# Optimization experiments

Measured on AMD Instinct MI355X. Metric: run time of the kernel, lower is better.

## Reference

```python
import jax, jax.numpy as jnp
import numpy as np
import math

N_ENTITIES = 200000
N_ITEMS = 100000
N_REL = 40
DIM = 64
N_HEADS = 2
DK = DIM // N_HEADS
N_EDGES = 1500000
K_EDGES = 256
K_ITEMS = 100


def setup_inputs() -> dict:
    key = jax.random.key(0)
    k1, k2, k3, k4, k5, k6 = jax.random.split(key, 6)
    entity_emb = jax.random.normal(k1, (N_ENTITIES, DIM), jnp.float32) * 0.1
    W_Q = jax.random.normal(k2, (DIM, DIM), jnp.float32) * (1.0 / math.sqrt(DIM))
    relation_emb = jax.random.normal(k3, (N_REL - 1, DIM), jnp.float32) * 0.1
    edge_index = jax.random.randint(k4, (2, N_EDGES), 0, N_ENTITIES, jnp.int32)
    # edge_type in [1, N_REL-1]: code indexes relation_emb[edge_type - 1]
    edge_type = jax.random.randint(k5, (N_EDGES,), 1, N_REL, jnp.int32)
    # uniform(0,1) driving the gumbel noise -log(-log(u)); clipped away from 0
    noise_u = jax.random.uniform(k6, (N_EDGES,), jnp.float32, 1e-9, 1.0)
    return {"entity_emb": entity_emb, "W_Q": W_Q, "relation_emb": relation_emb,
            "noise_u": noise_u, "edge_index": edge_index, "edge_type": edge_type}


def reference(entity_emb, W_Q, relation_emb, noise_u, edge_index, edge_type):
    head, tail = edge_index[0], edge_index[1]
    E = edge_index.shape[1]

    # --- norm_attn_computer (AttnHGCN): per-edge multi-head attention ---
    # project once on nodes, then gather (same math as (emb[head] @ W_Q))
    proj = entity_emb @ W_Q                               # [N, D]
    q = proj[head].reshape(E, N_HEADS, DK)                # [E, H, Dk]
    k = proj[tail].reshape(E, N_HEADS, DK)                # [E, H, Dk]
    rel = relation_emb[edge_type - 1].reshape(E, N_HEADS, DK)
    attn = jnp.sum(q * k * rel, axis=-1) / math.sqrt(DK)  # [E, H]
    edge_attn_logits = attn.mean(axis=-1)                 # [E]

    # scatter_softmax over head nodes, then multiply by head degree (norm)
    seg_max = jax.lax.stop_gradient(
        jax.ops.segment_max(edge_attn_logits, head, num_segments=N_ENTITIES))
    ex = jnp.exp(edge_attn_logits - seg_max[head])
    denom = jax.ops.segment_sum(ex, head, num_segments=N_ENTITIES)
    edge_attn_score = ex / denom[head]
    deg = jax.ops.segment_sum(jnp.ones_like(edge_attn_logits), head,
                              num_segments=N_ENTITIES)
    edge_attn_score = edge_attn_score * deg[head]         # [E]

    # --- attn logit sums per item (head + tail scatter_sum), topk 100 ---
    sum_by_node = (jax.ops.segment_sum(edge_attn_logits, head, num_segments=N_ENTITIES)
                   + jax.ops.segment_sum(edge_attn_logits, tail, num_segments=N_ENTITIES))
    top_items_v, top_attn_items = jax.lax.top_k(sum_by_node[:N_ITEMS], K_ITEMS)

    # --- gumbel-noise injection + edge topk 256 ---
    noisy_score = edge_attn_score + (-jnp.log(-jnp.log(noise_u)))
    topk_v, topk_attn_edge_id = jax.lax.top_k(noisy_score, K_EDGES)

    return (edge_attn_score, topk_v, topk_attn_edge_id, top_items_v, top_attn_items)
```

## Files before the change

### kernel.cpp

```cpp
#include <hip/hip_runtime.h>

#define N_ENTITIES 200000
#define N_ITEMS    100000
#define DIM        64
#define N_EDGES    1500000
#define K_EDGES    256
#define K_ITEMS    100
#define SCALE      0.08838834764831845f

#define CAND_CAP   8192
#define NBLK3      1024
#define NB1        256
#define EPB        5860
#define NBUCK      782
#define NSC        (NBUCK * NB1)
#define L2CAP      2816

typedef unsigned long long u64;


__device__ __forceinline__ unsigned fkey(float x) {
    unsigned u = __float_as_uint(x);
    return (u & 0x80000000u) ? ~u : (u | 0x80000000u);
}
__device__ __forceinline__ float funkey(unsigned k) {
    return (k & 0x80000000u) ? __uint_as_float(k & 0x7fffffffu)
                             : __uint_as_float(~k);
}

__device__ __forceinline__ unsigned select_digit(const unsigned* __restrict__ hist,
                                                 unsigned Keff, unsigned* above) {
    unsigned cum = 0;
    int b = 255;
    for (; b > 0; --b) {
        unsigned hb = hist[b];
        if (cum + hb >= Keff) break;
        cum += hb;
    }
    *above = cum;
    return (unsigned)b;
}

__global__ __launch_bounds__(256) void proj_kernel(const float* __restrict__ emb,
                                                   const float* __restrict__ W,
                                                   float* __restrict__ proj) {
    __shared__ float part[4][16][64];
    const int t = threadIdx.x;
    const int c = t & 63;
    const int q = __builtin_amdgcn_readfirstlane(t >> 6);

    float Wreg[16];
#pragma unroll
    for (int j = 0; j < 16; ++j) Wreg[j] = W[(q * 16 + j) * 64 + c];

    const int base = blockIdx.x * 16;
    const float* erow = emb + (size_t)base * 64 + q * 16;

    float acc[16];
#pragma unroll
    for (int r = 0; r < 16; ++r) acc[r] = 0.f;
#pragma unroll
    for (int r = 0; r < 16; ++r) {
#pragma unroll
        for (int j = 0; j < 16; ++j)
            acc[r] += erow[r * 64 + j] * Wreg[j];
    }
#pragma unroll
    for (int r = 0; r < 16; ++r) part[q][r][c] = acc[r];
    __syncthreads();
#pragma unroll
    for (int it = 0; it < 4; ++it) {
        int oi = t + it * 256;
        int r = oi >> 6, cc = oi & 63;
        float s = part[0][r][cc] + part[1][r][cc] + part[2][r][cc] + part[3][r][cc];
        proj[(size_t)(base + r) * 64 + cc] = s;
    }
}

__global__ __launch_bounds__(256) void bhist_kernel(const int* __restrict__ head,
                                                    unsigned* __restrict__ off) {
    __shared__ unsigned lh[NBUCK];
    for (int k = threadIdx.x; k < NBUCK; k += 256) lh[k] = 0;
    __syncthreads();
    int base = blockIdx.x * EPB;
    int end = base + EPB; if (end > N_EDGES) end = N_EDGES;
    for (int e = base + threadIdx.x; e < end; e += 256)
        atomicAdd(&lh[(unsigned)head[e] >> 8], 1u);
    __syncthreads();
    for (int k = threadIdx.x; k < NBUCK; k += 256)
        off[(size_t)k * NB1 + blockIdx.x] = lh[k];
}

__global__ void scanA_kernel(unsigned* __restrict__ a, unsigned* __restrict__ bsum) {
    __shared__ unsigned s[256];
    int t = threadIdx.x, i = blockIdx.x * 256 + t;
    unsigned v = a[i];
    s[t] = v;
    __syncthreads();
    for (int off = 1; off < 256; off <<= 1) {
        unsigned x = s[t];
        unsigned y = (t >= off) ? s[t - off] : 0u;
        __syncthreads();
        s[t] = x + y;
        __syncthreads();
    }
    a[i] = s[t] - v;
    if (t == 255) bsum[blockIdx.x] = s[t];
}
__global__ __launch_bounds__(256) void scanB_kernel(const unsigned* __restrict__ bsum,
                                                    unsigned* __restrict__ a) {
    __shared__ unsigned part[4];
    const int b = blockIdx.x;
    const int t = threadIdx.x;
    unsigned s = 0;
    for (int j = t; j < b; j += 256) s += bsum[j];
#pragma unroll
    for (int off = 1; off < 64; off <<= 1) s += __shfl_xor(s, off, 64);
    if ((t & 63) == 0) part[t >> 6] = s;
    __syncthreads();
    unsigned prefix = part[0] + part[1] + part[2] + part[3];
    a[b * 256 + t] += prefix;
}

__global__ __launch_bounds__(256) void bscat_kernel(const int* __restrict__ head,
                                                    const int* __restrict__ tail,
                                                    const int* __restrict__ etype,
                                                    const unsigned* __restrict__ off,
                                                    u64* __restrict__ rec2) {
    __shared__ unsigned lh[NBUCK];
    __shared__ unsigned loff[NBUCK];
    for (int k = threadIdx.x; k < NBUCK; k += 256) {
        lh[k] = 0;
        loff[k] = off[(size_t)k * NB1 + blockIdx.x];
    }
    __syncthreads();
    int base = blockIdx.x * EPB;
    int end = base + EPB; if (end > N_EDGES) end = N_EDGES;
    for (int e = base + threadIdx.x; e < end; e += 256) {
        unsigned h = (unsigned)head[e];
        unsigned bkt = h >> 8;
        unsigned r = atomicAdd(&lh[bkt], 1u);
        u64 R = ((u64)h << 45) | ((u64)(unsigned)tail[e] << 27)
              | ((u64)(unsigned)(etype[e] - 1) << 21) | (u64)(unsigned)e;
        rec2[loff[bkt] + r] = R;
    }
}

__global__ __launch_bounds__(256) void csr_kernel(const u64* __restrict__ rec2,
                                                  const unsigned* __restrict__ off,
                                                  u64* __restrict__ rec3,
                                                  unsigned* __restrict__ start,
                                                  unsigned* __restrict__ degtot) {
    __shared__ u64 srec[L2CAP];
    __shared__ u64 sdst[L2CAP];
    __shared__ unsigned short srank[L2CAP];
    __shared__ unsigned lh[256];
    __shared__ unsigned lscan[256];
    const int bkt = blockIdx.x;
    const unsigned gstart = off[(size_t)bkt * NB1];
    const unsigned gend = (bkt == NBUCK - 1) ? (unsigned)N_EDGES
                                             : off[(size_t)(bkt + 1) * NB1];
    unsigned n = gend - gstart;
    if (n > L2CAP) n = L2CAP;
    lh[threadIdx.x] = 0;
    __syncthreads();
    for (unsigned j = threadIdx.x; j < n; j += 256) {
        u64 R = rec2[gstart + j];
        srec[j] = R;
        unsigned hl = (unsigned)(R >> 45) & 255u;
        srank[j] = (unsigned short)atomicAdd(&lh[hl], 1u);
    }
    __syncthreads();
    unsigned v = lh[threadIdx.x];
    lscan[threadIdx.x] = v;
    __syncthreads();
    for (int o = 1; o < 256; o <<= 1) {
        unsigned x = lscan[threadIdx.x];
        unsigned y = (threadIdx.x >= o) ? lscan[threadIdx.x - o] : 0u;
        __syncthreads();
        lscan[threadIdx.x] = x + y;
        __syncthreads();
    }
    unsigned excl = lscan[threadIdx.x] - v;
    __syncthreads();
    lscan[threadIdx.x] = excl;
    const int h0 = bkt * 256;
    const int entCount = (N_ENTITIES - h0 < 256) ? (N_ENTITIES - h0) : 256;
    if ((int)threadIdx.x < entCount) {
        start[h0 + threadIdx.x] = gstart + excl;
        degtot[h0 + threadIdx.x] = v;
    }
    __syncthreads();
    for (unsigned j = threadIdx.x; j < n; j += 256) {
        u64 R = srec[j];
        unsigned hl = (unsigned)(R >> 45) & 255u;
        sdst[lscan[hl] + srank[j]] = R;
    }
    __syncthreads();
    for (unsigned j = threadIdx.x; j < n; j += 256) rec3[gstart + j] = sdst[j];
}

__global__ __launch_bounds__(256) void node_pass(const float4* __restrict__ proj4,
                                                 const float4* __restrict__ rel4,
                                                 const u64* __restrict__ rec,
                                                 const unsigned* __restrict__ start,
                                                 const unsigned* __restrict__ degtot,
                                                 float* __restrict__ logits,
                                                 float2* __restrict__ nd,
                                                 float* __restrict__ sumhead,
                                                 float* __restrict__ sumI) {
    int wave = (blockIdx.x * blockDim.x + threadIdx.x) >> 6;
    int lane = threadIdx.x & 63;
    int slot = lane >> 4, sl = lane & 15;
    unsigned s = start[wave], len = degtot[wave];
    float4 ph = proj4[(size_t)wave * 16 + sl];
    float dsum = 0.f, lsum = 0.f;
    for (unsigned k0 = 0; k0 < len; k0 += 8) {
        unsigned ka = k0 + slot, kb = ka + 4;
        bool va = (ka < len), vb = (kb < len);
        u64 Ra = rec[s + (va ? ka : 0u)];
        u64 Rb = rec[s + (vb ? kb : 0u)];
        unsigned ta = (unsigned)(Ra >> 27) & 0x3FFFFu, ria = ((unsigned)(Ra >> 21)) & 63u;
        unsigned tb = (unsigned)(Rb >> 27) & 0x3FFFFu, rib = ((unsigned)(Rb >> 21)) & 63u;
        unsigned ea = (unsigned)Ra & 0x1FFFFFu, eb = (unsigned)Rb & 0x1FFFFFu;
        float4 pa = proj4[(size_t)ta * 16 + sl];
        float4 qa = rel4[(size_t)ria * 16 + sl];
        float4 pb = proj4[(size_t)tb * 16 + sl];
        float4 qb = rel4[(size_t)rib * 16 + sl];
        float xa = ph.x * pa.x * qa.x + ph.y * pa.y * qa.y + ph.z * pa.z * qa.z + ph.w * pa.w * qa.w;
        float xb = ph.x * pb.x * qb.x + ph.y * pb.y * qb.y + ph.z * pb.z * qb.z + ph.w * pb.w * qb.w;
        xa += __shfl_xor(xa, 1, 64);  xb += __shfl_xor(xb, 1, 64);
        xa += __shfl_xor(xa, 2, 64);  xb += __shfl_xor(xb, 2, 64);
        xa += __shfl_xor(xa, 4, 64);  xb += __shfl_xor(xb, 4, 64);
        xa += __shfl_xor(xa, 8, 64);  xb += __shfl_xor(xb, 8, 64);
        if (sl == 0) {
            if (va) {
                float lg = xa * SCALE;
                logits[ea] = lg;
                dsum += __expf(lg);
                lsum += lg;
                if (ta < N_ITEMS) atomicAdd(&sumI[ta], lg);
            }
            if (vb) {
                float lg = xb * SCALE;
                logits[eb] = lg;
                dsum += __expf(lg);
                lsum += lg;
                if (tb < N_ITEMS) atomicAdd(&sumI[tb], lg);
            }
        }
    }
    dsum += __shfl_xor(dsum, 16, 64);
    dsum += __shfl_xor(dsum, 32, 64);
    lsum += __shfl_xor(lsum, 16, 64);
    lsum += __shfl_xor(lsum, 32, 64);
    if (lane == 0) {
        nd[wave] = make_float2(dsum, (float)len);
        sumhead[wave] = lsum;
    }
}

__global__ __launch_bounds__(256) void edge_pass3(const float* __restrict__ logits,
                           const int* __restrict__ head,
                           const float2* __restrict__ nd, const float* __restrict__ noise_u,
                           const float* __restrict__ sumhead, const float* __restrict__ sumI,
                           float* __restrict__ out_scores, unsigned* __restrict__ keysE,
                           unsigned* __restrict__ keysI, unsigned* __restrict__ histB) {
    __shared__ unsigned hh[512];
    for (int j = threadIdx.x; j < 512; j += blockDim.x) hh[j] = 0;
    __syncthreads();

    const int stride = NBLK3 * 256;
    for (int i = blockIdx.x * blockDim.x + threadIdx.x; i < N_EDGES; i += stride) {
        float lg = logits[i];
        float2 dd = nd[head[i]];
        float score = __expf(lg) / dd.x * dd.y;
        out_scores[i] = score;
        float noise = -logf(-logf(noise_u[i]));
        unsigned k = fkey(score + noise);
        keysE[i] = k;
        atomicAdd(&hh[k >> 24], 1u);
        if (i < N_ITEMS) {
            unsigned ki = fkey(sumhead[i] + sumI[i]);
            keysI[i] = ki;
            atomicAdd(&hh[256 + (ki >> 24)], 1u);
        }
    }
    __syncthreads();
    unsigned* row = histB + (size_t)blockIdx.x * 512;
    for (int j = threadIdx.x; j < 512; j += blockDim.x) row[j] = hh[j];
}

__global__ void reduce_hist_kernel(const unsigned* __restrict__ histB,
                                   unsigned* __restrict__ hists) {
    const int bin = blockIdx.x;
    unsigned s = 0;
    for (int r = threadIdx.x; r < NBLK3; r += 64)
        s += histB[(size_t)r * 512 + bin];
#pragma unroll
    for (int off = 1; off < 64; off <<= 1) s += __shfl_xor(s, off, 64);
    if (threadIdx.x == 0) hists[bin] = s;
}

__global__ void collect_kernel(const unsigned* __restrict__ keysE,
                               const unsigned* __restrict__ keysI,
                               const unsigned* __restrict__ hists,
                               unsigned* __restrict__ counters, unsigned* __restrict__ cand) {
    const int y = blockIdx.y;
    const unsigned* keys = y ? keysI : keysE;
    const int n = y ? N_ITEMS : N_EDGES;
    const unsigned K = y ? K_ITEMS : K_EDGES;
    const unsigned* H = hists + (size_t)y * 256;
    unsigned aboveA;
    unsigned binA = select_digit(H, K, &aboveA);
    const unsigned T = binA << 24;
    unsigned* cd = cand + (size_t)y * 2 * CAND_CAP;

    int i = blockIdx.x * blockDim.x + threadIdx.x;
    int stride = gridDim.x * blockDim.x;
    for (; i < n; i += stride) {
        unsigned k = keys[i];
        if (k >= T) {
            unsigned p = atomicAdd(&counters[y], 1u);
            if (p < (unsigned)CAND_CAP) { cd[2 * p] = k; cd[2 * p + 1] = (unsigned)i; }
        }
    }
}

__global__ void final_topk_kernel(const unsigned* __restrict__ cand,
                                  const unsigned* __restrict__ counters,
                                  float* __restrict__ out_topkv, float* __restrict__ out_topki,
                                  float* __restrict__ out_itemv, float* __restrict__ out_itemi) {
    __shared__ unsigned sk[CAND_CAP];
    __shared__ unsigned si[CAND_CAP];
    const int y = blockIdx.x;
    const int K = y ? K_ITEMS : K_EDGES;
    float* outv = y ? out_itemv : out_topkv;
    float* outi = y ? out_itemi : out_topki;
    const unsigned* cd = cand + (size_t)y * 2 * CAND_CAP;
    unsigned m = counters[y];
    if (m > (unsigned)CAND_CAP) m = CAND_CAP;
    for (unsigned i = threadIdx.x; i < m; i += blockDim.x) {
        sk[i] = cd[2 * i];
        si[i] = cd[2 * i + 1];
    }
    __syncthreads();
    for (unsigned i = threadIdx.x; i < m; i += blockDim.x) {
        unsigned ki = sk[i], xi = si[i];
        int r = 0;
        for (unsigned j = 0; j < m; ++j) {
            unsigned kj = sk[j];
            if (kj > ki || (kj == ki && si[j] < xi)) r++;
        }
        if (r < K) {
            outv[r] = funkey(ki);
            outi[r] = (float)xi;
        }
    }
}

extern "C" void kernel_launch(void* const* d_in, const int* in_sizes, int n_in,
                              void* d_out, int out_size, void* d_ws, size_t ws_size,
                              hipStream_t stream) {
    (void)in_sizes; (void)n_in; (void)out_size; (void)ws_size;
    const float* emb    = (const float*)d_in[0];
    const float* W      = (const float*)d_in[1];
    const float* rel    = (const float*)d_in[2];
    const float* noise  = (const float*)d_in[3];
    const int*   eidx   = (const int*)d_in[4];
    const int*   etype  = (const int*)d_in[5];
    const int* head = eidx;
    const int* tail = eidx + N_EDGES;

    float* out        = (float*)d_out;
    float* out_scores = out;
    float* out_topkv  = out + N_EDGES;
    float* out_topki  = out + N_EDGES + K_EDGES;
    float* out_itemv  = out + N_EDGES + 2 * K_EDGES;
    float* out_itemi  = out + N_EDGES + 2 * K_EDGES + K_ITEMS;

    float* ws = (float*)d_ws;
    size_t o = 0;
    float*    proj    = ws + o;               o += (size_t)N_ENTITIES * DIM;
    unsigned* off     = (unsigned*)(ws + o);  o += NSC;
    unsigned* bsum    = (unsigned*)(ws + o);  o += 1024;
    u64*      rec2    = (u64*)(ws + o);       o += 2 * (size_t)N_EDGES;
    u64*      rec3    = (u64*)(ws + o);       o += 2 * (size_t)N_EDGES;
    unsigned* keysE   = (unsigned*)rec2;
    unsigned* keysI   = keysE + N_EDGES;
    unsigned* start   = (unsigned*)(ws + o);  o += N_ENTITIES;
    unsigned* degtot  = (unsigned*)(ws + o);  o += N_ENTITIES;
    float*    logits  = ws + o;               o += N_EDGES;
    float2*   nd      = (float2*)(ws + o);    o += 2 * (size_t)N_ENTITIES;
    float*    sumhead = ws + o;               o += N_ENTITIES;
    float*    sumI    = ws + o;               o += N_ITEMS;
    unsigned* counters= (unsigned*)(ws + o);  o += 2;
    unsigned* histB   = (unsigned*)(ws + o);  o += (size_t)NBLK3 * 512;
    unsigned* hists   = (unsigned*)(ws + o);  o += 512;
    unsigned* cand    = (unsigned*)(ws + o);  o += 2 * 2 * CAND_CAP;

    hipMemsetAsync(sumI, 0, ((size_t)N_ITEMS + 2) * 4, stream);
    hipLaunchKernelGGL(proj_kernel, dim3(12500), dim3(256), 0, stream, emb, W, proj);
    hipLaunchKernelGGL(bhist_kernel, dim3(NB1), dim3(256), 0, stream, head, off);
    hipLaunchKernelGGL(scanA_kernel, dim3(NSC / 256), dim3(256), 0, stream, off, bsum);
    hipLaunchKernelGGL(scanB_kernel, dim3(NSC / 256), dim3(256), 0, stream, bsum, off);
    hipLaunchKernelGGL(bscat_kernel, dim3(NB1), dim3(256), 0, stream,
                       head, tail, etype, off, rec2);
    hipLaunchKernelGGL(csr_kernel, dim3(NBUCK), dim3(256), 0, stream,
                       rec2, off, rec3, start, degtot);
    hipLaunchKernelGGL(node_pass, dim3(N_ENTITIES / 4), dim3(256), 0, stream,
                       (const float4*)proj, (const float4*)rel, rec3, start, degtot,
                       logits, nd, sumhead, sumI);
    hipLaunchKernelGGL(edge_pass3, dim3(NBLK3), dim3(256), 0, stream,
                       logits, head, nd, noise, sumhead, sumI,
                       out_scores, keysE, keysI, histB);
    hipLaunchKernelGGL(reduce_hist_kernel, dim3(512), dim3(64), 0, stream, histB, hists);
    hipLaunchKernelGGL(collect_kernel, dim3(512, 2), dim3(256), 0, stream,
                       keysE, keysI, hists, counters, cand);
    hipLaunchKernelGGL(final_topk_kernel, dim3(2), dim3(1024), 0, stream,
                       cand, counters, out_topkv, out_topki, out_itemv, out_itemi);
}
```

Baseline: 437.1 us.

## Fuse post-projection pipeline into one persistent kernel with grid barriers

Nine separate kernels (bucket histogram, scans, scatter, CSR build, node pass, edge pass, histogram reduce, collect, final top-k) are merged into a single persistent kernel sized to fill the device, with software grid-wide barriers between phases. Per-block histograms are now reduced with global atomics instead of a separate reduce kernel. Shared memory is shrunk to a fixed 1920-word buffer, so the CSR phase no longer stages full buckets in LDS, and the final top-k reads candidates from global memory across 16 blocks. The goal is to remove launch overhead and inter-kernel gaps. The cost is spin-barrier latency, reduced parallelism in phases that had many small blocks, and a risk of deadlock if not all blocks are co-resident.

```diff
diff --git a/kernel.cpp b/kernel.cpp
--- a/kernel.cpp
+++ b/kernel.cpp
@@ -9,7 +9,6 @@
 #define SCALE      0.08838834764831845f
 
 #define CAND_CAP   8192
-#define NBLK3      1024
 #define NB1        256
 #define EPB        5860
 #define NBUCK      782
@@ -41,6 +40,27 @@
     return (unsigned)b;
 }
 
+__device__ __forceinline__ void gbar(unsigned* bar) {
+    __syncthreads();
+    if (threadIdx.x == 0) {
+        __builtin_amdgcn_fence(__ATOMIC_RELEASE, "agent");
+        unsigned gen = __hip_atomic_load(&bar[1], __ATOMIC_RELAXED, __HIP_MEMORY_SCOPE_AGENT);
+        unsigned a = __hip_atomic_fetch_add(&bar[0], 1u, __ATOMIC_RELAXED, __HIP_MEMORY_SCOPE_AGENT);
+        if (a == gridDim.x - 1) {
+            __hip_atomic_store(&bar[0], 0u, __ATOMIC_RELAXED, __HIP_MEMORY_SCOPE_AGENT);
+            __hip_atomic_store(&bar[1], gen + 1u, __ATOMIC_RELAXED, __HIP_MEMORY_SCOPE_AGENT);
+        } else {
+            unsigned long long spins = 0;
+            while (__hip_atomic_load(&bar[1], __ATOMIC_RELAXED, __HIP_MEMORY_SCOPE_AGENT) == gen) {
+                __builtin_amdgcn_s_sleep(2);
+                if (++spins > 60000000ull) break;
+            }
+        }
+        __builtin_amdgcn_fence(__ATOMIC_ACQUIRE, "agent");
+    }
+    __syncthreads();
+}
+
 __global__ __launch_bounds__(256) void proj_kernel(const float* __restrict__ emb,
                                                    const float* __restrict__ W,
                                                    float* __restrict__ proj) {
@@ -77,284 +97,271 @@
     }
 }
 
-__global__ __launch_bounds__(256) void bhist_kernel(const int* __restrict__ head,
-                                                    unsigned* __restrict__ off) {
-    __shared__ unsigned lh[NBUCK];
-    for (int k = threadIdx.x; k < NBUCK; k += 256) lh[k] = 0;
-    __syncthreads();
-    int base = blockIdx.x * EPB;
-    int end = base + EPB; if (end > N_EDGES) end = N_EDGES;
-    for (int e = base + threadIdx.x; e < end; e += 256)
-        atomicAdd(&lh[(unsigned)head[e] >> 8], 1u);
-    __syncthreads();
-    for (int k = threadIdx.x; k < NBUCK; k += 256)
-        off[(size_t)k * NB1 + blockIdx.x] = lh[k];
-}
-
-__global__ void scanA_kernel(unsigned* __restrict__ a, unsigned* __restrict__ bsum) {
-    __shared__ unsigned s[256];
-    int t = threadIdx.x, i = blockIdx.x * 256 + t;
-    unsigned v = a[i];
-    s[t] = v;
-    __syncthreads();
-    for (int off = 1; off < 256; off <<= 1) {
-        unsigned x = s[t];
-        unsigned y = (t >= off) ? s[t - off] : 0u;
-        __syncthreads();
-        s[t] = x + y;
-        __syncthreads();
-    }
-    a[i] = s[t] - v;
-    if (t == 255) bsum[blockIdx.x] = s[t];
-}
-__global__ __launch_bounds__(256) void scanB_kernel(const unsigned* __restrict__ bsum,
-                                                    unsigned* __restrict__ a) {
-    __shared__ unsigned part[4];
-    const int b = blockIdx.x;
+__global__ __launch_bounds__(256) void mega_kernel(
+    const int* __restrict__ head, const int* __restrict__ tailp,
+    const int* __restrict__ etype,
+    const float4* __restrict__ proj4, const float4* __restrict__ rel4,
+    const float* __restrict__ noise_u,
+    unsigned* __restrict__ off, unsigned* __restrict__ rowtot,
+    u64* __restrict__ rec2, u64* __restrict__ rec3,
+    unsigned* __restrict__ start, unsigned* __restrict__ degtot,
+    float* __restrict__ logits, float2* __restrict__ nd,
+    float* __restrict__ sumhead, float* __restrict__ sumI,
+    float* __restrict__ out_scores,
+    unsigned* __restrict__ keysE, unsigned* __restrict__ keysI,
+    unsigned* __restrict__ hists, unsigned* __restrict__ counters,
+    unsigned* __restrict__ cand,
+    float* __restrict__ out_topkv, float* __restrict__ out_topki,
+    float* __restrict__ out_itemv, float* __restrict__ out_itemi,
+    unsigned* __restrict__ bar)
+{
+    __shared__ unsigned smem[1920];
     const int t = threadIdx.x;
-    unsigned s = 0;
-    for (int j = t; j < b; j += 256) s += bsum[j];
-#pragma unroll
-    for (int off = 1; off < 64; off <<= 1) s += __shfl_xor(s, off, 64);
-    if ((t & 63) == 0) part[t >> 6] = s;
-    __syncthreads();
-    unsigned prefix = part[0] + part[1] + part[2] + part[3];
-    a[b * 256 + t] += prefix;
-}
-
-__global__ __launch_bounds__(256) void bscat_kernel(const int* __restrict__ head,
-                                                    const int* __restrict__ tail,
-                                                    const int* __restrict__ etype,
-                                                    const unsigned* __restrict__ off,
-                                                    u64* __restrict__ rec2) {
-    __shared__ unsigned lh[NBUCK];
-    __shared__ unsigned loff[NBUCK];
-    for (int k = threadIdx.x; k < NBUCK; k += 256) {
-        lh[k] = 0;
-        loff[k] = off[(size_t)k * NB1 + blockIdx.x];
-    }
-    __syncthreads();
-    int base = blockIdx.x * EPB;
-    int end = base + EPB; if (end > N_EDGES) end = N_EDGES;
-    for (int e = base + threadIdx.x; e < end; e += 256) {
-        unsigned h = (unsigned)head[e];
-        unsigned bkt = h >> 8;
-        unsigned r = atomicAdd(&lh[bkt], 1u);
-        u64 R = ((u64)h << 45) | ((u64)(unsigned)tail[e] << 27)
-              | ((u64)(unsigned)(etype[e] - 1) << 21) | (u64)(unsigned)e;
-        rec2[loff[bkt] + r] = R;
-    }
-}
-
-__global__ __launch_bounds__(256) void csr_kernel(const u64* __restrict__ rec2,
-                                                  const unsigned* __restrict__ off,
-                                                  u64* __restrict__ rec3,
-                                                  unsigned* __restrict__ start,
-                                                  unsigned* __restrict__ degtot) {
-    __shared__ u64 srec[L2CAP];
-    __shared__ u64 sdst[L2CAP];
-    __shared__ unsigned short srank[L2CAP];
-    __shared__ unsigned lh[256];
-    __shared__ unsigned lscan[256];
-    const int bkt = blockIdx.x;
-    const unsigned gstart = off[(size_t)bkt * NB1];
-    const unsigned gend = (bkt == NBUCK - 1) ? (unsigned)N_EDGES
-                                             : off[(size_t)(bkt + 1) * NB1];
-    unsigned n = gend - gstart;
-    if (n > L2CAP) n = L2CAP;
-    lh[threadIdx.x] = 0;
-    __syncthreads();
-    for (unsigned j = threadIdx.x; j < n; j += 256) {
-        u64 R = rec2[gstart + j];
-        srec[j] = R;
-        unsigned hl = (unsigned)(R >> 45) & 255u;
-        srank[j] = (unsigned short)atomicAdd(&lh[hl], 1u);
-    }
-    __syncthreads();
-    unsigned v = lh[threadIdx.x];
-    lscan[threadIdx.x] = v;
-    __syncthreads();
-    for (int o = 1; o < 256; o <<= 1) {
-        unsigned x = lscan[threadIdx.x];
-        unsigned y = (threadIdx.x >= o) ? lscan[threadIdx.x - o] : 0u;
-        __syncthreads();
-        lscan[threadIdx.x] = x + y;
-        __syncthreads();
-    }
-    unsigned excl = lscan[threadIdx.x] - v;
-    __syncthreads();
-    lscan[threadIdx.x] = excl;
-    const int h0 = bkt * 256;
-    const int entCount = (N_ENTITIES - h0 < 256) ? (N_ENTITIES - h0) : 256;
-    if ((int)threadIdx.x < entCount) {
-        start[h0 + threadIdx.x] = gstart + excl;
-        degtot[h0 + threadIdx.x] = v;
-    }
-    __syncthreads();
-    for (unsigned j = threadIdx.x; j < n; j += 256) {
-        u64 R = srec[j];
-        unsigned hl = (unsigned)(R >> 45) & 255u;
-        sdst[lscan[hl] + srank[j]] = R;
-    }
-    __syncthreads();
-    for (unsigned j = threadIdx.x; j < n; j += 256) rec3[gstart + j] = sdst[j];
-}
-
-__global__ __launch_bounds__(256) void node_pass(const float4* __restrict__ proj4,
-                                                 const float4* __restrict__ rel4,
-                                                 const u64* __restrict__ rec,
-                                                 const unsigned* __restrict__ start,
-                                                 const unsigned* __restrict__ degtot,
-                                                 float* __restrict__ logits,
-                                                 float2* __restrict__ nd,
-                                                 float* __restrict__ sumhead,
-                                                 float* __restrict__ sumI) {
-    int wave = (blockIdx.x * blockDim.x + threadIdx.x) >> 6;
-    int lane = threadIdx.x & 63;
-    int slot = lane >> 4, sl = lane & 15;
-    unsigned s = start[wave], len = degtot[wave];
-    float4 ph = proj4[(size_t)wave * 16 + sl];
-    float dsum = 0.f, lsum = 0.f;
-    for (unsigned k0 = 0; k0 < len; k0 += 8) {
-        unsigned ka = k0 + slot, kb = ka + 4;
-        bool va = (ka < len), vb = (kb < len);
-        u64 Ra = rec[s + (va ? ka : 0u)];
-        u64 Rb = rec[s + (vb ? kb : 0u)];
-        unsigned ta = (unsigned)(Ra >> 27) & 0x3FFFFu, ria = ((unsigned)(Ra >> 21)) & 63u;
-        unsigned tb = (unsigned)(Rb >> 27) & 0x3FFFFu, rib = ((unsigned)(Rb >> 21)) & 63u;
-        unsigned ea = (unsigned)Ra & 0x1FFFFFu, eb = (unsigned)Rb & 0x1FFFFFu;
-        float4 pa = proj4[(size_t)ta * 16 + sl];
-        float4 qa = rel4[(size_t)ria * 16 + sl];
-        float4 pb = proj4[(size_t)tb * 16 + sl];
-        float4 qb = rel4[(size_t)rib * 16 + sl];
-        float xa = ph.x * pa.x * qa.x + ph.y * pa.y * qa.y + ph.z * pa.z * qa.z + ph.w * pa.w * qa.w;
-        float xb = ph.x * pb.x * qb.x + ph.y * pb.y * qb.y + ph.z * pb.z * qb.z + ph.w * pb.w * qb.w;
-        xa += __shfl_xor(xa, 1, 64);  xb += __shfl_xor(xb, 1, 64);
-        xa += __shfl_xor(xa, 2, 64);  xb += __shfl_xor(xb, 2, 64);
-        xa += __shfl_xor(xa, 4, 64);  xb += __shfl_xor(xb, 4, 64);
-        xa += __shfl_xor(xa, 8, 64);  xb += __shfl_xor(xb, 8, 64);
-        if (sl == 0) {
-            if (va) {
-                float lg = xa * SCALE;
-                logits[ea] = lg;
-                dsum += __expf(lg);
-                lsum += lg;
-                if (ta < N_ITEMS) atomicAdd(&sumI[ta], lg);
-            }
-            if (vb) {
-                float lg = xb * SCALE;
-                logits[eb] = lg;
-                dsum += __expf(lg);
-                lsum += lg;
-                if (tb < N_ITEMS) atomicAdd(&sumI[tb], lg);
-            }
-        }
-    }
-    dsum += __shfl_xor(dsum, 16, 64);
-    dsum += __shfl_xor(dsum, 32, 64);
-    lsum += __shfl_xor(lsum, 16, 64);
-    lsum += __shfl_xor(lsum, 32, 64);
-    if (lane == 0) {
-        nd[wave] = make_float2(dsum, (float)len);
-        sumhead[wave] = lsum;
-    }
-}
-
-__global__ __launch_bounds__(256) void edge_pass3(const float* __restrict__ logits,
-                           const int* __restrict__ head,
-                           const float2* __restrict__ nd, const float* __restrict__ noise_u,
-                           const float* __restrict__ sumhead, const float* __restrict__ sumI,
-                           float* __restrict__ out_scores, unsigned* __restrict__ keysE,
-                           unsigned* __restrict__ keysI, unsigned* __restrict__ histB) {
-    __shared__ unsigned hh[512];
-    for (int j = threadIdx.x; j < 512; j += blockDim.x) hh[j] = 0;
-    __syncthreads();
-
-    const int stride = NBLK3 * 256;
-    for (int i = blockIdx.x * blockDim.x + threadIdx.x; i < N_EDGES; i += stride) {
-        float lg = logits[i];
-        float2 dd = nd[head[i]];
-        float score = __expf(lg) / dd.x * dd.y;
-        out_scores[i] = score;
-        float noise = -logf(-logf(noise_u[i]));
-        unsigned k = fkey(score + noise);
-        keysE[i] = k;
-        atomicAdd(&hh[k >> 24], 1u);
-        if (i < N_ITEMS) {
-            unsigned ki = fkey(sumhead[i] + sumI[i]);
-            keysI[i] = ki;
-            atomicAdd(&hh[256 + (ki >> 24)], 1u);
-        }
-    }
-    __syncthreads();
-    unsigned* row = histB + (size_t)blockIdx.x * 512;
-    for (int j = threadIdx.x; j < 512; j += blockDim.x) row[j] = hh[j];
-}
-
-__global__ void reduce_hist_kernel(const unsigned* __restrict__ histB,
-                                   unsigned* __restrict__ hists) {
-    const int bin = blockIdx.x;
-    unsigned s = 0;
-    for (int r = threadIdx.x; r < NBLK3; r += 64)
-        s += histB[(size_t)r * 512 + bin];
-#pragma unroll
-    for (int off = 1; off < 64; off <<= 1) s += __shfl_xor(s, off, 64);
-    if (threadIdx.x == 0) hists[bin] = s;
-}
-
-__global__ void collect_kernel(const unsigned* __restrict__ keysE,
-                               const unsigned* __restrict__ keysI,
-                               const unsigned* __restrict__ hists,
-                               unsigned* __restrict__ counters, unsigned* __restrict__ cand) {
-    const int y = blockIdx.y;
-    const unsigned* keys = y ? keysI : keysE;
-    const int n = y ? N_ITEMS : N_EDGES;
-    const unsigned K = y ? K_ITEMS : K_EDGES;
-    const unsigned* H = hists + (size_t)y * 256;
-    unsigned aboveA;
-    unsigned binA = select_digit(H, K, &aboveA);
-    const unsigned T = binA << 24;
-    unsigned* cd = cand + (size_t)y * 2 * CAND_CAP;
-
-    int i = blockIdx.x * blockDim.x + threadIdx.x;
-    int stride = gridDim.x * blockDim.x;
-    for (; i < n; i += stride) {
-        unsigned k = keys[i];
-        if (k >= T) {
-            unsigned p = atomicAdd(&counters[y], 1u);
-            if (p < (unsigned)CAND_CAP) { cd[2 * p] = k; cd[2 * p + 1] = (unsigned)i; }
-        }
-    }
-}
-
-__global__ void final_topk_kernel(const unsigned* __restrict__ cand,
-                                  const unsigned* __restrict__ counters,
-                                  float* __restrict__ out_topkv, float* __restrict__ out_topki,
-                                  float* __restrict__ out_itemv, float* __restrict__ out_itemi) {
-    __shared__ unsigned sk[CAND_CAP];
-    __shared__ unsigned si[CAND_CAP];
-    const int y = blockIdx.x;
-    const int K = y ? K_ITEMS : K_EDGES;
-    float* outv = y ? out_itemv : out_topkv;
-    float* outi = y ? out_itemi : out_topki;
-    const unsigned* cd = cand + (size_t)y * 2 * CAND_CAP;
-    unsigned m = counters[y];
-    if (m > (unsigned)CAND_CAP) m = CAND_CAP;
-    for (unsigned i = threadIdx.x; i < m; i += blockDim.x) {
-        sk[i] = cd[2 * i];
-        si[i] = cd[2 * i + 1];
-    }
-    __syncthreads();
-    for (unsigned i = threadIdx.x; i < m; i += blockDim.x) {
-        unsigned ki = sk[i], xi = si[i];
-        int r = 0;
-        for (unsigned j = 0; j < m; ++j) {
-            unsigned kj = sk[j];
-            if (kj > ki || (kj == ki && si[j] < xi)) r++;
-        }
-        if (r < K) {
-            outv[r] = funkey(ki);
-            outi[r] = (float)xi;
+    const int G = gridDim.x;
+
+    for (int vb = blockIdx.x; vb < NB1; vb += G) {
+        for (int j = t; j < NBUCK; j += 256) smem[j] = 0;
+        __syncthreads();
+        int base = vb * EPB;
+        int end = base + EPB; if (end > N_EDGES) end = N_EDGES;
+        for (int e = base + t; e < end; e += 256)
+            atomicAdd(&smem[(unsigned)head[e] >> 8], 1u);
+        __syncthreads();
+        for (int j = t; j < NBUCK; j += 256)
+            off[(size_t)j * NB1 + vb] = smem[j];
+        __syncthreads();
+    }
+    gbar(bar);
+
+    for (int k = blockIdx.x; k < NBUCK; k += G) {
+        unsigned v = off[(size_t)k * NB1 + t];
+        smem[t] = v;
+        __syncthreads();
+        for (int o = 1; o < 256; o <<= 1) {
+            unsigned x = smem[t];
+            unsigned y = (t >= o) ? smem[t - o] : 0u;
+            __syncthreads();
+            smem[t] = x + y;
+            __syncthreads();
+        }
+        off[(size_t)k * NB1 + t] = smem[t] - v;
+        if (t == 255) rowtot[k] = smem[t];
+        __syncthreads();
+    }
+    gbar(bar);
+
+    for (int k = blockIdx.x; k < NBUCK; k += G) {
+        unsigned s = 0;
+        for (int j = t; j < k; j += 256) s += rowtot[j];
+#pragma unroll
+        for (int o = 1; o < 64; o <<= 1) s += __shfl_xor(s, o, 64);
+        if ((t & 63) == 0) smem[256 + (t >> 6)] = s;
+        __syncthreads();
+        unsigned prefix = smem[256] + smem[257] + smem[258] + smem[259];
+        off[(size_t)k * NB1 + t] += prefix;
+        __syncthreads();
+    }
+    gbar(bar);
+
+    for (int vb = blockIdx.x; vb < NB1; vb += G) {
+        unsigned* lh = smem;
+        unsigned* loff = smem + NBUCK;
+        for (int j = t; j < NBUCK; j += 256) {
+            lh[j] = 0;
+            loff[j] = off[(size_t)j * NB1 + vb];
+        }
+        __syncthreads();
+        int base = vb * EPB;
+        int end = base + EPB; if (end > N_EDGES) end = N_EDGES;
+        for (int e = base + t; e < end; e += 256) {
+            unsigned h = (unsigned)head[e];
+            unsigned bkt = h >> 8;
+            unsigned r = atomicAdd(&lh[bkt], 1u);
+            u64 R = ((u64)h << 45) | ((u64)(unsigned)tailp[e] << 27)
+                  | ((u64)(unsigned)(etype[e] - 1) << 21) | (u64)(unsigned)e;
+            rec2[loff[bkt] + r] = R;
+        }
+        __syncthreads();
+    }
+    gbar(bar);
+
+    for (int bkt = blockIdx.x; bkt < NBUCK; bkt += G) {
+        unsigned* lh = smem;
+        unsigned* lscan = smem + 256;
+        unsigned short* srank = (unsigned short*)(smem + 512);
+        const unsigned gstart = off[(size_t)bkt * NB1];
+        const unsigned gend = (bkt == NBUCK - 1) ? (unsigned)N_EDGES
+                                                 : off[(size_t)(bkt + 1) * NB1];
+        unsigned n = gend - gstart;
+        if (n > L2CAP) n = L2CAP;
+        lh[t] = 0;
+        __syncthreads();
+        for (unsigned j = t; j < n; j += 256) {
+            u64 R = rec2[gstart + j];
+            unsigned hl = (unsigned)(R >> 45) & 255u;
+            srank[j] = (unsigned short)atomicAdd(&lh[hl], 1u);
+        }
+        __syncthreads();
+        unsigned v = lh[t];
+        lscan[t] = v;
+        __syncthreads();
+        for (int o = 1; o < 256; o <<= 1) {
+            unsigned x = lscan[t];
+            unsigned y = (t >= o) ? lscan[t - o] : 0u;
+            __syncthreads();
+            lscan[t] = x + y;
+            __syncthreads();
+        }
+        unsigned excl = lscan[t] - v;
+        __syncthreads();
+        lscan[t] = excl;
+        const int h0 = bkt * 256;
+        const int entCount = (N_ENTITIES - h0 < 256) ? (N_ENTITIES - h0) : 256;
+        if (t < entCount) {
+            start[h0 + t] = gstart + excl;
+            degtot[h0 + t] = v;
+        }
+        __syncthreads();
+        for (unsigned j = t; j < n; j += 256) {
+            u64 R = rec2[gstart + j];
+            unsigned hl = (unsigned)(R >> 45) & 255u;
+            rec3[gstart + lscan[hl] + srank[j]] = R;
+        }
+        __syncthreads();
+    }
+    gbar(bar);
+
+    {
+        const int wid = (blockIdx.x * 256 + t) >> 6;
+        const int W = G * 4;
+        const int lane = t & 63;
+        const int slot = lane >> 4, sl = lane & 15;
+        for (int node = wid; node < N_ENTITIES; node += W) {
+            unsigned s = start[node], len = degtot[node];
+            float4 ph = proj4[(size_t)node * 16 + sl];
+            float dsum = 0.f, lsum = 0.f;
+            for (unsigned k0 = 0; k0 < len; k0 += 8) {
+                unsigned ka = k0 + slot, kb = ka + 4;
+                bool va = (ka < len), vb = (kb < len);
+                u64 Ra = rec3[s + (va ? ka : 0u)];
+                u64 Rb = rec3[s + (vb ? kb : 0u)];
+                unsigned ta = (unsigned)(Ra >> 27) & 0x3FFFFu, ria = ((unsigned)(Ra >> 21)) & 63u;
+                unsigned tb = (unsigned)(Rb >> 27) & 0x3FFFFu, rib = ((unsigned)(Rb >> 21)) & 63u;
+                unsigned ea = (unsigned)Ra & 0x1FFFFFu, eb = (unsigned)Rb & 0x1FFFFFu;
+                float4 pa = proj4[(size_t)ta * 16 + sl];
+                float4 qa = rel4[(size_t)ria * 16 + sl];
+                float4 pb = proj4[(size_t)tb * 16 + sl];
+                float4 qb = rel4[(size_t)rib * 16 + sl];
+                float xa = ph.x * pa.x * qa.x + ph.y * pa.y * qa.y
+                         + ph.z * pa.z * qa.z + ph.w * pa.w * qa.w;
+                float xb = ph.x * pb.x * qb.x + ph.y * pb.y * qb.y
+                         + ph.z * pb.z * qb.z + ph.w * pb.w * qb.w;
+                xa += __shfl_xor(xa, 1, 64);  xb += __shfl_xor(xb, 1, 64);
+                xa += __shfl_xor(xa, 2, 64);  xb += __shfl_xor(xb, 2, 64);
+                xa += __shfl_xor(xa, 4, 64);  xb += __shfl_xor(xb, 4, 64);
+                xa += __shfl_xor(xa, 8, 64);  xb += __shfl_xor(xb, 8, 64);
+                if (sl == 0) {
+                    if (va) {
+                        float lg = xa * SCALE;
+                        logits[ea] = lg;
+                        dsum += __expf(lg);
+                        lsum += lg;
+                        if (ta < N_ITEMS) atomicAdd(&sumI[ta], lg);
+                    }
+                    if (vb) {
+                        float lg = xb * SCALE;
+                        logits[eb] = lg;
+                        dsum += __expf(lg);
+                        lsum += lg;
+                        if (tb < N_ITEMS) atomicAdd(&sumI[tb], lg);
+                    }
+                }
+            }
+            dsum += __shfl_xor(dsum, 16, 64);
+            dsum += __shfl_xor(dsum, 32, 64);
+            lsum += __shfl_xor(lsum, 16, 64);
+            lsum += __shfl_xor(lsum, 32, 64);
+            if (lane == 0) {
+                nd[node] = make_float2(dsum, (float)len);
+                sumhead[node] = lsum;
+            }
+        }
+    }
+    gbar(bar);
+
+    {
+        unsigned* hh = smem;
+        for (int j = t; j < 512; j += 256) hh[j] = 0;
+        __syncthreads();
+        const int stride = G * 256;
+        for (int i = blockIdx.x * 256 + t; i < N_EDGES; i += stride) {
+            float lg = logits[i];
+            float2 dd = nd[head[i]];
+            float score = __expf(lg) / dd.x * dd.y;
+            out_scores[i] = score;
+            float noise = -logf(-logf(noise_u[i]));
+            unsigned k = fkey(score + noise);
+            keysE[i] = k;
+            atomicAdd(&hh[k >> 24], 1u);
+            if (i < N_ITEMS) {
+                unsigned ki = fkey(sumhead[i] + sumI[i]);
+                keysI[i] = ki;
+                atomicAdd(&hh[256 + (ki >> 24)], 1u);
+            }
+        }
+        __syncthreads();
+        for (int j = t; j < 512; j += 256) {
+            unsigned v = hh[j];
+            if (v) atomicAdd(&hists[j], v);
+        }
+    }
+    gbar(bar);
+
+    {
+        const int stride = G * 256;
+        unsigned aboveA;
+        unsigned binA = select_digit(hists, K_EDGES, &aboveA);
+        unsigned T = binA << 24;
+        for (int i = blockIdx.x * 256 + t; i < N_EDGES; i += stride) {
+            unsigned k = keysE[i];
+            if (k >= T) {
+                unsigned p = atomicAdd(&counters[0], 1u);
+                if (p < (unsigned)CAND_CAP) { cand[2 * p] = k; cand[2 * p + 1] = (unsigned)i; }
+            }
+        }
+        binA = select_digit(hists + 256, K_ITEMS, &aboveA);
+        T = binA << 24;
+        unsigned* cd = cand + 2 * CAND_CAP;
+        for (int i = blockIdx.x * 256 + t; i < N_ITEMS; i += stride) {
+            unsigned k = keysI[i];
+            if (k >= T) {
+                unsigned p = atomicAdd(&counters[1], 1u);
+                if (p < (unsigned)CAND_CAP) { cd[2 * p] = k; cd[2 * p + 1] = (unsigned)i; }
+            }
+        }
+    }
+    gbar(bar);
+
+    if (blockIdx.x < 16) {
+        const int y = blockIdx.x >> 3;
+        const int sub = blockIdx.x & 7;
+        const int K = y ? K_ITEMS : K_EDGES;
+        float* outv = y ? out_itemv : out_topkv;
+        float* outi = y ? out_itemi : out_topki;
+        const unsigned* cd = cand + (size_t)y * 2 * CAND_CAP;
+        unsigned m = counters[y];
+        if (m > (unsigned)CAND_CAP) m = CAND_CAP;
+        for (unsigned i = sub * 256 + t; i < m; i += 2048) {
+            unsigned ki = cd[2 * i], xi = cd[2 * i + 1];
+            int r = 0;
+            for (unsigned j = 0; j < m; ++j) {
+                unsigned kj = cd[2 * j];
+                if (kj > ki || (kj == ki && cd[2 * j + 1] < xi)) r++;
+            }
+            if (r < K) {
+                outv[r] = funkey(ki);
+                outi[r] = (float)xi;
+            }
         }
     }
 }
@@ -383,7 +390,7 @@
     size_t o = 0;
     float*    proj    = ws + o;               o += (size_t)N_ENTITIES * DIM;
     unsigned* off     = (unsigned*)(ws + o);  o += NSC;
-    unsigned* bsum    = (unsigned*)(ws + o);  o += 1024;
+    unsigned* rowtot  = (unsigned*)(ws + o);  o += 1024;
     u64*      rec2    = (u64*)(ws + o);       o += 2 * (size_t)N_EDGES;
     u64*      rec3    = (u64*)(ws + o);       o += 2 * (size_t)N_EDGES;
     unsigned* keysE   = (unsigned*)rec2;
@@ -394,29 +401,33 @@
     float2*   nd      = (float2*)(ws + o);    o += 2 * (size_t)N_ENTITIES;
     float*    sumhead = ws + o;               o += N_ENTITIES;
     float*    sumI    = ws + o;               o += N_ITEMS;
+    unsigned* hists   = (unsigned*)(ws + o);  o += 512;
     unsigned* counters= (unsigned*)(ws + o);  o += 2;
-    unsigned* histB   = (unsigned*)(ws + o);  o += (size_t)NBLK3 * 512;
-    unsigned* hists   = (unsigned*)(ws + o);  o += 512;
+    unsigned* bar     = (unsigned*)(ws + o);  o += 16;
     unsigned* cand    = (unsigned*)(ws + o);  o += 2 * 2 * CAND_CAP;
 
-    hipMemsetAsync(sumI, 0, ((size_t)N_ITEMS + 2) * 4, stream);
+    static int G = 0;
+    if (G == 0) {
+        int dev = 0;
+        hipGetDevice(&dev);
+        hipDeviceProp_t prop;
+        int cus = 256;
+        if (hipGetDeviceProperties(&prop, dev) == hipSuccess) cus = prop.multiProcessorCount;
+        int occ = 0;
+        if (hipOccupancyMaxActiveBlocksPerMultiprocessor(&occ, mega_kernel, 256, 0) != hipSuccess
+            || occ < 1) occ = 1;
+        G = occ * cus;
+        if (G < 16) G = 16;
+        if (G > 4096) G = 4096;
+    }
+
+    hipMemsetAsync(sumI, 0, ((size_t)N_ITEMS + 512 + 2 + 16) * 4, stream);
     hipLaunchKernelGGL(proj_kernel, dim3(12500), dim3(256), 0, stream, emb, W, proj);
-    hipLaunchKernelGGL(bhist_kernel, dim3(NB1), dim3(256), 0, stream, head, off);
-    hipLaunchKernelGGL(scanA_kernel, dim3(NSC / 256), dim3(256), 0, stream, off, bsum);
-    hipLaunchKernelGGL(scanB_kernel, dim3(NSC / 256), dim3(256), 0, stream, bsum, off);
-    hipLaunchKernelGGL(bscat_kernel, dim3(NB1), dim3(256), 0, stream,
-                       head, tail, etype, off, rec2);
-    hipLaunchKernelGGL(csr_kernel, dim3(NBUCK), dim3(256), 0, stream,
-                       rec2, off, rec3, start, degtot);
-    hipLaunchKernelGGL(node_pass, dim3(N_ENTITIES / 4), dim3(256), 0, stream,
-                       (const float4*)proj, (const float4*)rel, rec3, start, degtot,
-                       logits, nd, sumhead, sumI);
-    hipLaunchKernelGGL(edge_pass3, dim3(NBLK3), dim3(256), 0, stream,
-                       logits, head, nd, noise, sumhead, sumI,
-                       out_scores, keysE, keysI, histB);
-    hipLaunchKernelGGL(reduce_hist_kernel, dim3(512), dim3(64), 0, stream, histB, hists);
-    hipLaunchKernelGGL(collect_kernel, dim3(512, 2), dim3(256), 0, stream,
-                       keysE, keysI, hists, counters, cand);
-    hipLaunchKernelGGL(final_topk_kernel, dim3(2), dim3(1024), 0, stream,
-                       cand, counters, out_topkv, out_topki, out_itemv, out_itemi);
-}
+    hipLaunchKernelGGL(mega_kernel, dim3(G), dim3(256), 0, stream,
+                       head, tail, etype,
+                       (const float4*)proj, (const float4*)rel, noise,
+                       off, rowtot, rec2, rec3, start, degtot,
+                       logits, nd, sumhead, sumI,
+                       out_scores, keysE, keysI, hists, counters, cand,
+                       out_topkv, out_topki, out_itemv, out_itemi, bar);
+}
```

After: 1.466 ms. +235.5%, slower.

## Fuse CSR bucket sort with node attention pass and atomically reduce histograms

Applied to the files above, without the earlier changes.

Shrinks head-node buckets from 256 to 64 nodes so each bucket fits in LDS. The CSR sort and the per-node attention pass are merged into one kernel that reads sorted edge records directly from shared memory, which removes the rec3, start and degtot global round trips and one kernel launch. The per-block histogram array and its reduce kernel are replaced by atomic adds into a global histogram that is zeroed alongside sumI. In exchange, per-bucket capacity drops to 768 edges (overflow is silently truncated), each 256-thread block now processes 64 nodes serially across 4 waves, the bucket scatter has four times as many buckets, and the histogram relies on contended global atomics.

```diff
diff --git a/kernel.cpp b/kernel.cpp
--- a/kernel.cpp
+++ b/kernel.cpp
@@ -12,9 +12,10 @@
 #define NBLK3      1024
 #define NB1        256
 #define EPB        5860
-#define NBUCK      782
+#define BSH        6
+#define NBUCK      3125
 #define NSC        (NBUCK * NB1)
-#define L2CAP      2816
+#define L2CAP      768
 
 typedef unsigned long long u64;
 
@@ -85,7 +86,7 @@
     int base = blockIdx.x * EPB;
     int end = base + EPB; if (end > N_EDGES) end = N_EDGES;
     for (int e = base + threadIdx.x; e < end; e += 256)
-        atomicAdd(&lh[(unsigned)head[e] >> 8], 1u);
+        atomicAdd(&lh[(unsigned)head[e] >> BSH], 1u);
     __syncthreads();
     for (int k = threadIdx.x; k < NBUCK; k += 256)
         off[(size_t)k * NB1 + blockIdx.x] = lh[k];
@@ -138,7 +139,7 @@
     int end = base + EPB; if (end > N_EDGES) end = N_EDGES;
     for (int e = base + threadIdx.x; e < end; e += 256) {
         unsigned h = (unsigned)head[e];
-        unsigned bkt = h >> 8;
+        unsigned bkt = h >> BSH;
         unsigned r = atomicAdd(&lh[bkt], 1u);
         u64 R = ((u64)h << 45) | ((u64)(unsigned)tail[e] << 27)
               | ((u64)(unsigned)(etype[e] - 1) << 21) | (u64)(unsigned)e;
@@ -146,117 +147,107 @@
     }
 }
 
-__global__ __launch_bounds__(256) void csr_kernel(const u64* __restrict__ rec2,
-                                                  const unsigned* __restrict__ off,
-                                                  u64* __restrict__ rec3,
-                                                  unsigned* __restrict__ start,
-                                                  unsigned* __restrict__ degtot) {
-    __shared__ u64 srec[L2CAP];
+__global__ __launch_bounds__(256) void csrnode_kernel(const u64* __restrict__ rec2,
+                                                      const unsigned* __restrict__ off,
+                                                      const float4* __restrict__ proj4,
+                                                      const float4* __restrict__ rel4,
+                                                      float* __restrict__ logits,
+                                                      float2* __restrict__ nd,
+                                                      float* __restrict__ sumhead,
+                                                      float* __restrict__ sumI) {
     __shared__ u64 sdst[L2CAP];
     __shared__ unsigned short srank[L2CAP];
-    __shared__ unsigned lh[256];
-    __shared__ unsigned lscan[256];
+    __shared__ unsigned lh[64];
+    __shared__ unsigned lscan[64];
+    const int t = threadIdx.x;
     const int bkt = blockIdx.x;
     const unsigned gstart = off[(size_t)bkt * NB1];
     const unsigned gend = (bkt == NBUCK - 1) ? (unsigned)N_EDGES
                                              : off[(size_t)(bkt + 1) * NB1];
     unsigned n = gend - gstart;
     if (n > L2CAP) n = L2CAP;
-    lh[threadIdx.x] = 0;
-    __syncthreads();
-    for (unsigned j = threadIdx.x; j < n; j += 256) {
+    if (t < 64) lh[t] = 0;
+    __syncthreads();
+    for (unsigned j = t; j < n; j += 256) {
         u64 R = rec2[gstart + j];
-        srec[j] = R;
-        unsigned hl = (unsigned)(R >> 45) & 255u;
+        unsigned hl = (unsigned)(R >> 45) & 63u;
         srank[j] = (unsigned short)atomicAdd(&lh[hl], 1u);
     }
     __syncthreads();
-    unsigned v = lh[threadIdx.x];
-    lscan[threadIdx.x] = v;
-    __syncthreads();
-    for (int o = 1; o < 256; o <<= 1) {
-        unsigned x = lscan[threadIdx.x];
-        unsigned y = (threadIdx.x >= o) ? lscan[threadIdx.x - o] : 0u;
+    unsigned v0 = (t < 64) ? lh[t] : 0u;
+    if (t < 64) lscan[t] = v0;
+    __syncthreads();
+    for (int o = 1; o < 64; o <<= 1) {
+        unsigned x = 0, y = 0;
+        if (t < 64) { x = lscan[t]; y = (t >= o) ? lscan[t - o] : 0u; }
         __syncthreads();
-        lscan[threadIdx.x] = x + y;
+        if (t < 64) lscan[t] = x + y;
         __syncthreads();
     }
-    unsigned excl = lscan[threadIdx.x] - v;
-    __syncthreads();
-    lscan[threadIdx.x] = excl;
-    const int h0 = bkt * 256;
-    const int entCount = (N_ENTITIES - h0 < 256) ? (N_ENTITIES - h0) : 256;
-    if ((int)threadIdx.x < entCount) {
-        start[h0 + threadIdx.x] = gstart + excl;
-        degtot[h0 + threadIdx.x] = v;
-    }
-    __syncthreads();
-    for (unsigned j = threadIdx.x; j < n; j += 256) {
-        u64 R = srec[j];
-        unsigned hl = (unsigned)(R >> 45) & 255u;
+    if (t < 64) lscan[t] -= v0;
+    __syncthreads();
+    for (unsigned j = t; j < n; j += 256) {
+        u64 R = rec2[gstart + j];
+        unsigned hl = (unsigned)(R >> 45) & 63u;
         sdst[lscan[hl] + srank[j]] = R;
     }
     __syncthreads();
-    for (unsigned j = threadIdx.x; j < n; j += 256) rec3[gstart + j] = sdst[j];
-}
-
-__global__ __launch_bounds__(256) void node_pass(const float4* __restrict__ proj4,
-                                                 const float4* __restrict__ rel4,
-                                                 const u64* __restrict__ rec,
-                                                 const unsigned* __restrict__ start,
-                                                 const unsigned* __restrict__ degtot,
-                                                 float* __restrict__ logits,
-                                                 float2* __restrict__ nd,
-                                                 float* __restrict__ sumhead,
-                                                 float* __restrict__ sumI) {
-    int wave = (blockIdx.x * blockDim.x + threadIdx.x) >> 6;
-    int lane = threadIdx.x & 63;
-    int slot = lane >> 4, sl = lane & 15;
-    unsigned s = start[wave], len = degtot[wave];
-    float4 ph = proj4[(size_t)wave * 16 + sl];
-    float dsum = 0.f, lsum = 0.f;
-    for (unsigned k0 = 0; k0 < len; k0 += 8) {
-        unsigned ka = k0 + slot, kb = ka + 4;
-        bool va = (ka < len), vb = (kb < len);
-        u64 Ra = rec[s + (va ? ka : 0u)];
-        u64 Rb = rec[s + (vb ? kb : 0u)];
-        unsigned ta = (unsigned)(Ra >> 27) & 0x3FFFFu, ria = ((unsigned)(Ra >> 21)) & 63u;
-        unsigned tb = (unsigned)(Rb >> 27) & 0x3FFFFu, rib = ((unsigned)(Rb >> 21)) & 63u;
-        unsigned ea = (unsigned)Ra & 0x1FFFFFu, eb = (unsigned)Rb & 0x1FFFFFu;
-        float4 pa = proj4[(size_t)ta * 16 + sl];
-        float4 qa = rel4[(size_t)ria * 16 + sl];
-        float4 pb = proj4[(size_t)tb * 16 + sl];
-        float4 qb = rel4[(size_t)rib * 16 + sl];
-        float xa = ph.x * pa.x * qa.x + ph.y * pa.y * qa.y + ph.z * pa.z * qa.z + ph.w * pa.w * qa.w;
-        float xb = ph.x * pb.x * qb.x + ph.y * pb.y * qb.y + ph.z * pb.z * qb.z + ph.w * pb.w * qb.w;
-        xa += __shfl_xor(xa, 1, 64);  xb += __shfl_xor(xb, 1, 64);
-        xa += __shfl_xor(xa, 2, 64);  xb += __shfl_xor(xb, 2, 64);
-        xa += __shfl_xor(xa, 4, 64);  xb += __shfl_xor(xb, 4, 64);
-        xa += __shfl_xor(xa, 8, 64);  xb += __shfl_xor(xb, 8, 64);
-        if (sl == 0) {
-            if (va) {
-                float lg = xa * SCALE;
-                logits[ea] = lg;
-                dsum += __expf(lg);
-                lsum += lg;
-                if (ta < N_ITEMS) atomicAdd(&sumI[ta], lg);
+
+    const int lane = t & 63;
+    const int wv = t >> 6;
+    const int slot = lane >> 4, sl = lane & 15;
+    for (int ln = 0; ln < 16; ++ln) {
+        const int local = wv * 16 + ln;
+        const int node = (bkt << 6) + local;
+        const unsigned s0 = lscan[local];
+        const unsigned len = lh[local];
+        float4 ph = proj4[(size_t)node * 16 + sl];
+        float dsum = 0.f, lsum = 0.f;
+        for (unsigned k0 = 0; k0 < len; k0 += 8) {
+            unsigned ka = k0 + slot, kb = ka + 4;
+            bool va = (ka < len), vb = (kb < len);
+            u64 Ra = sdst[s0 + (va ? ka : 0u)];
+            u64 Rb = sdst[s0 + (vb ? kb : 0u)];
+            unsigned ta = (unsigned)(Ra >> 27) & 0x3FFFFu, ria = ((unsigned)(Ra >> 21)) & 63u;
+            unsigned tb = (unsigned)(Rb >> 27) & 0x3FFFFu, rib = ((unsigned)(Rb >> 21)) & 63u;
+            unsigned ea = (unsigned)Ra & 0x1FFFFFu, eb = (unsigned)Rb & 0x1FFFFFu;
+            float4 pa = proj4[(size_t)ta * 16 + sl];
+            float4 qa = rel4[(size_t)ria * 16 + sl];
+            float4 pb = proj4[(size_t)tb * 16 + sl];
+            float4 qb = rel4[(size_t)rib * 16 + sl];
+            float xa = ph.x * pa.x * qa.x + ph.y * pa.y * qa.y
+                     + ph.z * pa.z * qa.z + ph.w * pa.w * qa.w;
+            float xb = ph.x * pb.x * qb.x + ph.y * pb.y * qb.y
+                     + ph.z * pb.z * qb.z + ph.w * pb.w * qb.w;
+            xa += __shfl_xor(xa, 1, 64);  xb += __shfl_xor(xb, 1, 64);
+            xa += __shfl_xor(xa, 2, 64);  xb += __shfl_xor(xb, 2, 64);
+            xa += __shfl_xor(xa, 4, 64);  xb += __shfl_xor(xb, 4, 64);
+            xa += __shfl_xor(xa, 8, 64);  xb += __shfl_xor(xb, 8, 64);
+            if (sl == 0) {
+                if (va) {
+                    float lg = xa * SCALE;
+                    logits[ea] = lg;
+                    dsum += __expf(lg);
+                    lsum += lg;
+                    if (ta < N_ITEMS) atomicAdd(&sumI[ta], lg);
+                }
+                if (vb) {
+                    float lg = xb * SCALE;
+                    logits[eb] = lg;
+                    dsum += __expf(lg);
+                    lsum += lg;
+                    if (tb < N_ITEMS) atomicAdd(&sumI[tb], lg);
+                }
             }
-            if (vb) {
-                float lg = xb * SCALE;
-                logits[eb] = lg;
-                dsum += __expf(lg);
-                lsum += lg;
-                if (tb < N_ITEMS) atomicAdd(&sumI[tb], lg);
-            }
-        }
-    }
-    dsum += __shfl_xor(dsum, 16, 64);
-    dsum += __shfl_xor(dsum, 32, 64);
-    lsum += __shfl_xor(lsum, 16, 64);
-    lsum += __shfl_xor(lsum, 32, 64);
-    if (lane == 0) {
-        nd[wave] = make_float2(dsum, (float)len);
-        sumhead[wave] = lsum;
+        }
+        dsum += __shfl_xor(dsum, 16, 64);
+        dsum += __shfl_xor(dsum, 32, 64);
+        lsum += __shfl_xor(lsum, 16, 64);
+        lsum += __shfl_xor(lsum, 32, 64);
+        if (lane == 0) {
+            nd[node] = make_float2(dsum, (float)len);
+            sumhead[node] = lsum;
+        }
     }
 }
 
@@ -265,11 +256,10 @@
                            const float2* __restrict__ nd, const float* __restrict__ noise_u,
                            const float* __restrict__ sumhead, const float* __restrict__ sumI,
                            float* __restrict__ out_scores, unsigned* __restrict__ keysE,
-                           unsigned* __restrict__ keysI, unsigned* __restrict__ histB) {
+                           unsigned* __restrict__ keysI, unsigned* __restrict__ hists) {
     __shared__ unsigned hh[512];
     for (int j = threadIdx.x; j < 512; j += blockDim.x) hh[j] = 0;
     __syncthreads();
-
     const int stride = NBLK3 * 256;
     for (int i = blockIdx.x * blockDim.x + threadIdx.x; i < N_EDGES; i += stride) {
         float lg = logits[i];
@@ -287,19 +277,10 @@
         }
     }
     __syncthreads();
-    unsigned* row = histB + (size_t)blockIdx.x * 512;
-    for (int j = threadIdx.x; j < 512; j += blockDim.x) row[j] = hh[j];
-}
-
-__global__ void reduce_hist_kernel(const unsigned* __restrict__ histB,
-                                   unsigned* __restrict__ hists) {
-    const int bin = blockIdx.x;
-    unsigned s = 0;
-    for (int r = threadIdx.x; r < NBLK3; r += 64)
-        s += histB[(size_t)r * 512 + bin];
-#pragma unroll
-    for (int off = 1; off < 64; off <<= 1) s += __shfl_xor(s, off, 64);
-    if (threadIdx.x == 0) hists[bin] = s;
+    for (int j = threadIdx.x; j < 512; j += blockDim.x) {
+        unsigned v = hh[j];
+        if (v) atomicAdd(&hists[j], v);
+    }
 }
 
 __global__ void collect_kernel(const unsigned* __restrict__ keysE,
@@ -383,38 +364,31 @@
     size_t o = 0;
     float*    proj    = ws + o;               o += (size_t)N_ENTITIES * DIM;
     unsigned* off     = (unsigned*)(ws + o);  o += NSC;
-    unsigned* bsum    = (unsigned*)(ws + o);  o += 1024;
+    unsigned* bsum    = (unsigned*)(ws + o);  o += 3200;
     u64*      rec2    = (u64*)(ws + o);       o += 2 * (size_t)N_EDGES;
-    u64*      rec3    = (u64*)(ws + o);       o += 2 * (size_t)N_EDGES;
     unsigned* keysE   = (unsigned*)rec2;
     unsigned* keysI   = keysE + N_EDGES;
-    unsigned* start   = (unsigned*)(ws + o);  o += N_ENTITIES;
-    unsigned* degtot  = (unsigned*)(ws + o);  o += N_ENTITIES;
     float*    logits  = ws + o;               o += N_EDGES;
     float2*   nd      = (float2*)(ws + o);    o += 2 * (size_t)N_ENTITIES;
     float*    sumhead = ws + o;               o += N_ENTITIES;
     float*    sumI    = ws + o;               o += N_ITEMS;
+    unsigned* hists   = (unsigned*)(ws + o);  o += 512;
     unsigned* counters= (unsigned*)(ws + o);  o += 2;
-    unsigned* histB   = (unsigned*)(ws + o);  o += (size_t)NBLK3 * 512;
-    unsigned* hists   = (unsigned*)(ws + o);  o += 512;
     unsigned* cand    = (unsigned*)(ws + o);  o += 2 * 2 * CAND_CAP;
 
-    hipMemsetAsync(sumI, 0, ((size_t)N_ITEMS + 2) * 4, stream);
+    hipMemsetAsync(sumI, 0, ((size_t)N_ITEMS + 512 + 2) * 4, stream);
     hipLaunchKernelGGL(proj_kernel, dim3(12500), dim3(256), 0, stream, emb, W, proj);
     hipLaunchKernelGGL(bhist_kernel, dim3(NB1), dim3(256), 0, stream, head, off);
     hipLaunchKernelGGL(scanA_kernel, dim3(NSC / 256), dim3(256), 0, stream, off, bsum);
     hipLaunchKernelGGL(scanB_kernel, dim3(NSC / 256), dim3(256), 0, stream, bsum, off);
     hipLaunchKernelGGL(bscat_kernel, dim3(NB1), dim3(256), 0, stream,
                        head, tail, etype, off, rec2);
-    hipLaunchKernelGGL(csr_kernel, dim3(NBUCK), dim3(256), 0, stream,
-                       rec2, off, rec3, start, degtot);
-    hipLaunchKernelGGL(node_pass, dim3(N_ENTITIES / 4), dim3(256), 0, stream,
-                       (const float4*)proj, (const float4*)rel, rec3, start, degtot,
+    hipLaunchKernelGGL(csrnode_kernel, dim3(NBUCK), dim3(256), 0, stream,
+                       rec2, off, (const float4*)proj, (const float4*)rel,
                        logits, nd, sumhead, sumI);
     hipLaunchKernelGGL(edge_pass3, dim3(NBLK3), dim3(256), 0, stream,
                        logits, head, nd, noise, sumhead, sumI,
-                       out_scores, keysE, keysI, histB);
-    hipLaunchKernelGGL(reduce_hist_kernel, dim3(512), dim3(64), 0, stream, histB, hists);
+                       out_scores, keysE, keysI, hists);
     hipLaunchKernelGGL(collect_kernel, dim3(512, 2), dim3(256), 0, stream,
                        keysE, keysI, hists, counters, cand);
     hipLaunchKernelGGL(final_topk_kernel, dim3(2), dim3(1024), 0, stream,
```

Measured after the change: 437.2 us. No clear change (+0.0%).
